# Kernel tuning notes

Measured on AMD Instinct MI355X. Metric: run time of the kernel, lower is better.

Reference implementation:

```python
import jax, jax.numpy as jnp
import numpy as np


def setup_inputs() -> dict:
    key = jax.random.key(0)
    k1, k2, k3 = jax.random.split(key, 3)
    B, C, H, W = 4, 32, 256, 256
    nw, nh = 16, 16
    K = nw * nh
    pixel_feats = jax.random.normal(k1, (B, C, H, W), dtype=jnp.float32)
    assoc_map = jax.random.uniform(k2, (B, 9, H, W), dtype=jnp.float32)
    index_map = jax.random.randint(k3, (B, H, W), 0, K, dtype=jnp.int32)
    return {
        "pixel_feats": pixel_feats,
        "assoc_map": assoc_map,
        "index_map": index_map,
        "nw_spixels": nw,
        "nh_spixels": nh,
    }


def reference(pixel_feats, assoc_map, index_map, nw_spixels, nh_spixels):
    # pixel_feats: [B,C,H,W], assoc_map: [B,9,H,W] (3x3 superpixel-neighbor
    # association weights, row-major (dy,dx) in {-1,0,1}^2), index_map: [B,H,W]
    # base superpixel id in [0, nw*nh). Output: [B, C, nw*nh].
    B, C, H, W = pixel_feats.shape
    K = nw_spixels * nh_spixels
    P = H * W

    idx = index_map.reshape(B, P).astype(jnp.int32)
    ix = idx % nw_spixels  # base spixel grid x
    iy = idx // nw_spixels  # base spixel grid y

    # 9 relative offsets over the superpixel grid
    dy, dx = jnp.meshgrid(jnp.arange(-1, 2), jnp.arange(-1, 2), indexing="ij")
    dy = dy.reshape(9)
    dx = dx.reshape(9)

    tx = ix[:, None, :] + dx[None, :, None]  # [B,9,P]
    ty = iy[:, None, :] + dy[None, :, None]
    valid = (tx >= 0) & (tx < nw_spixels) & (ty >= 0) & (ty < nh_spixels)
    tgt = jnp.where(valid, ty * nw_spixels + tx, 0)  # [B,9,P]

    w = assoc_map.reshape(B, 9, P) * valid.astype(assoc_map.dtype)  # [B,9,P]

    # fold batch into segment id so a single segment_sum handles all images
    seg = (tgt + jnp.arange(B, dtype=jnp.int32)[:, None, None] * K).reshape(-1)

    wsum = jax.ops.segment_sum(w.reshape(-1), seg, num_segments=B * K)  # [B*K]

    # weighted pixel features scattered into superpixel bins
    contrib = w[:, :, None, :] * pixel_feats.reshape(B, 1, C, P)  # [B,9,C,P]
    contrib = contrib.transpose(0, 1, 3, 2).reshape(-1, C)  # [B*9*P, C]
    fsum = jax.ops.segment_sum(contrib, seg, num_segments=B * K)  # [B*K, C]

    eps = 1e-16
    denom = jnp.where(wsum > eps, wsum, 1.0)
    sp = jnp.where(wsum[:, None] > eps, fsum / denom[:, None], 0.0)
    return sp.reshape(B, K, C).transpose(0, 2, 1)  # [B,C,K]
```

## Files before the change

kernel.cpp:

```cpp
#include <hip/hip_runtime.h>
#include <hip/hip_bf16.h>


#define CCH  32
#define TPB  1024
#define PPB  1024
#define STPB 512
#define CAPC 384
#define RECW 24
#define CNTS 16
#define KMAX 256

__device__ __forceinline__ unsigned pack_bf16(float a, float b) {
    unsigned ua = __float_as_uint(a);
    unsigned ub = __float_as_uint(b);
    ua = (ua + 0x7FFFu + ((ua >> 16) & 1u)) >> 16;
    ub = (ub + 0x7FFFu + ((ub >> 16) & 1u)) >> 16;
    return ua | (ub << 16);
}
__device__ __forceinline__ float bf_lo(unsigned u) {
    return __uint_as_float(u << 16);
}
__device__ __forceinline__ float bf_hi(unsigned u) {
    return __uint_as_float(u & 0xFFFF0000u);
}

__global__ __launch_bounds__(TPB) void spx_prep_kernel(
    const float* __restrict__ pf,
    const float* __restrict__ assoc,
    const int*   __restrict__ idxmap,
    const int*   __restrict__ nw_p,
    const int*   __restrict__ nh_p,
    int*         __restrict__ cnt,
    unsigned*    __restrict__ recs,
    float*       __restrict__ ovf,
    int P, int K, int cap, int bpb)
{
    __shared__ int hist[KMAX];
    __shared__ int bases[KMAX];

    const int b   = blockIdx.x / bpb;
    const int blk = blockIdx.x - b * bpb;
    const int tid = threadIdx.x;
    const int p   = blk * PPB + tid;

    if (tid < KMAX) hist[tid] = 0;
    __syncthreads();

    const int*   ix_b = idxmap + (size_t)b * P;
    const float* pf_b = pf     + (size_t)b * CCH * P;
    const float* as_b = assoc  + (size_t)b * 9 * P;

    const int idx  = ix_b[p];
    const int rank = atomicAdd(&hist[idx], 1);

    unsigned u[16];
#pragma unroll
    for (int c2 = 0; c2 < 16; ++c2) {
        const float f0 = pf_b[(size_t)(2*c2  ) * P + p];
        const float f1 = pf_b[(size_t)(2*c2+1) * P + p];
        u[c2] = pack_bf16(f0, f1);
    }
    float wv[9];
#pragma unroll
    for (int j = 0; j < 9; ++j) wv[j] = as_b[(size_t)j * P + p];

    __syncthreads();
    if (tid < KMAX)
        bases[tid] = atomicAdd(&cnt[(b * K + tid) * CNTS], hist[tid]);
    __syncthreads();

    const int pos = bases[idx] + rank;

    if (pos < cap) {
        unsigned* dst = recs + ((size_t)(b * K + idx) * cap + pos) * RECW;
        uint4* d4 = (uint4*)dst;
        d4[0] = make_uint4(u[0],  u[1],  u[2],  u[3]);
        d4[1] = make_uint4(u[4],  u[5],  u[6],  u[7]);
        d4[2] = make_uint4(u[8],  u[9],  u[10], u[11]);
        d4[3] = make_uint4(u[12], u[13], u[14], u[15]);
        d4[4] = make_uint4(pack_bf16(wv[0], wv[1]), pack_bf16(wv[2], wv[3]),
                           pack_bf16(wv[4], wv[5]), pack_bf16(wv[6], wv[7]));
        dst[20] = pack_bf16(wv[8], 0.0f);
    } else {
        const int nw = nw_p[0], nh = nh_p[0];
        const int iy = idx / nw, ixx = idx - (idx / nw) * nw;
#pragma unroll
        for (int j = 0; j < 9; ++j) {
            const int ty = iy + j / 3 - 1, tx = ixx + j % 3 - 1;
            if (tx >= 0 && tx < nw && ty >= 0 && ty < nh) {
                float* o = ovf + (size_t)(b * K + ty * nw + tx) * (CCH + 1);
#pragma unroll
                for (int c2 = 0; c2 < 16; ++c2) {
                    unsafeAtomicAdd(&o[2*c2],     wv[j] * bf_lo(u[c2]));
                    unsafeAtomicAdd(&o[2*c2 + 1], wv[j] * bf_hi(u[c2]));
                }
                unsafeAtomicAdd(&o[CCH], wv[j]);
            }
        }
    }
}

__global__ __launch_bounds__(STPB) void spx_scan_kernel(
    const unsigned* __restrict__ recs,
    const int*      __restrict__ cnt,
    float*          __restrict__ partial,
    int K, int cap)
{
    __shared__ float red[32][9][CCH + 1];

    const int bs  = blockIdx.x;
    const int tid = threadIdx.x;
    const int c2  = tid & 15;
    const int g   = tid >> 4;

    int c = cnt[bs * CNTS];
    if (c > cap) c = cap;
    const unsigned* rb = recs + (size_t)bs * cap * RECW;

    float a[9][2];
    float wa = 0.f;
#pragma unroll
    for (int j = 0; j < 9; ++j) { a[j][0] = 0.f; a[j][1] = 0.f; }

    for (int i = g; i < c; i += 32) {
        const unsigned* r = rb + (size_t)i * RECW;
        const unsigned uf  = r[c2];
        const float f0 = bf_lo(uf), f1 = bf_hi(uf);
        const unsigned wp0 = r[16], wp1 = r[17], wp2 = r[18],
                       wp3 = r[19], wp4 = r[20];
        const float w[9] = { bf_lo(wp0), bf_hi(wp0), bf_lo(wp1), bf_hi(wp1),
                             bf_lo(wp2), bf_hi(wp2), bf_lo(wp3), bf_hi(wp3),
                             bf_lo(wp4) };
#pragma unroll
        for (int j = 0; j < 9; ++j) {
            a[j][0] += w[j] * f0;
            a[j][1] += w[j] * f1;
        }
        wa += w[0] + w[1] + w[2] + w[3] + w[4] + w[5] + w[6] + w[7] + w[8];
    }

    (void)wa;

    float ws[9];
#pragma unroll
    for (int j = 0; j < 9; ++j) ws[j] = 0.f;
    if (c2 == 0) {
        for (int i = g; i < c; i += 32) {
            const unsigned* r = rb + (size_t)i * RECW;
            const unsigned wp0 = r[16], wp1 = r[17], wp2 = r[18],
                           wp3 = r[19], wp4 = r[20];
            ws[0] += bf_lo(wp0); ws[1] += bf_hi(wp0);
            ws[2] += bf_lo(wp1); ws[3] += bf_hi(wp1);
            ws[4] += bf_lo(wp2); ws[5] += bf_hi(wp2);
            ws[6] += bf_lo(wp3); ws[7] += bf_hi(wp3);
            ws[8] += bf_lo(wp4);
        }
    }

#pragma unroll
    for (int j = 0; j < 9; ++j) {
        red[g][j][2 * c2]     = a[j][0];
        red[g][j][2 * c2 + 1] = a[j][1];
    }
    if (c2 == 0) {
#pragma unroll
        for (int j = 0; j < 9; ++j) red[g][j][CCH] = ws[j];
    }
    __syncthreads();

    float* pout = partial + (size_t)bs * 9 * (CCH + 1);
    for (int col = tid; col < 9 * (CCH + 1); col += STPB) {
        const int j  = col / (CCH + 1);
        const int cc = col - j * (CCH + 1);
        float s = 0.f;
#pragma unroll
        for (int g2 = 0; g2 < 32; ++g2) s += red[g2][j][cc];
        pout[col] = s;
    }
}

__global__ __launch_bounds__(64) void spx_finalize_kernel(
    const float* __restrict__ partial,
    const float* __restrict__ ovf,
    const int*   __restrict__ nw_p,
    const int*   __restrict__ nh_p,
    float*       __restrict__ out,
    int K)
{
    __shared__ float F[CCH + 1];

    const int b   = blockIdx.x / K;
    const int k   = blockIdx.x - b * K;
    const int tid = threadIdx.x;
    const int nw  = nw_p[0];
    const int nh  = nh_p[0];
    const int ky  = k / nw;
    const int kx  = k - ky * nw;

    if (tid < CCH + 1) {
        float s = ovf[(size_t)(b * K + k) * (CCH + 1) + tid];
#pragma unroll
        for (int j = 0; j < 9; ++j) {
            const int dy = j / 3 - 1, dx = j % 3 - 1;
            const int sy = ky - dy, sx = kx - dx;
            if (sx >= 0 && sx < nw && sy >= 0 && sy < nh) {
                s += partial[((size_t)(b * K + sy * nw + sx) * 9 + j)
                             * (CCH + 1) + tid];
            }
        }
        F[tid] = s;
    }
    __syncthreads();

    if (tid < CCH) {
        const float W = F[CCH];
        out[((size_t)b * CCH + tid) * K + k] =
            (W > 1e-16f) ? (F[tid] / W) : 0.f;
    }
}

extern "C" void kernel_launch(void* const* d_in, const int* in_sizes, int n_in,
                              void* d_out, int out_size, void* d_ws, size_t ws_size,
                              hipStream_t stream) {
    const float* pf     = (const float*)d_in[0];
    const float* assoc  = (const float*)d_in[1];
    const int*   idxmap = (const int*)d_in[2];
    const int*   nw_p   = (const int*)d_in[3];
    const int*   nh_p   = (const int*)d_in[4];
    float* out = (float*)d_out;

    const int BP = in_sizes[2];
    const int B  = 4;
    const int P  = BP / B;
    const int K  = out_size / (B * CCH);

    const size_t cnt_bytes  = (size_t)B * K * CNTS * sizeof(int);
    const size_t ovf_bytes  = (size_t)B * K * (CCH + 1) * sizeof(float);
    const size_t part_bytes = (size_t)B * K * 9 * (CCH + 1) * sizeof(float);
    int*      cnt     = (int*)d_ws;
    float*    ovf     = (float*)((char*)d_ws + cnt_bytes);
    float*    partial = (float*)((char*)d_ws + cnt_bytes + ovf_bytes);
    unsigned* recs    = (unsigned*)((char*)d_ws + cnt_bytes + ovf_bytes
                                    + part_bytes);

    size_t used = cnt_bytes + ovf_bytes + part_bytes;
    size_t avail = (ws_size > used) ? (ws_size - used) : 0;
    int cap = (int)(avail / ((size_t)B * K * RECW * sizeof(unsigned)));
    if (cap > CAPC) cap = CAPC;
    if (cap < 1) cap = 1;

    hipMemsetAsync(cnt, 0, cnt_bytes + ovf_bytes, stream);

    const int bpb = P / PPB;
    spx_prep_kernel<<<B * bpb, TPB, 0, stream>>>(
        pf, assoc, idxmap, nw_p, nh_p, cnt, recs, ovf, P, K, cap, bpb);

    spx_scan_kernel<<<B * K, STPB, 0, stream>>>(recs, cnt, partial, K, cap);

    spx_finalize_kernel<<<B * K, 64, 0, stream>>>(
        partial, ovf, nw_p, nh_p, out, K);
}
```

Measured before the change: 112.4 us.

## Split prep into rank and fill kernels; fold weight sums into main scan loop

The combined prep kernel is split in two. A light 1024-thread rank kernel reads only the index map and computes each pixel's slot. A separate 256-thread fill kernel then loads features and weights and writes the bf16 records, so the heavy loads no longer sit inside a block that syncs twice. The scan kernel now accumulates the per-neighbor weight sums inside its main loop instead of rereading the records in a second pass on one lane per group. The split adds a kernel launch and a slot array round-trip through global memory. The overflow path now reloads fp32 features instead of using the packed bf16 values.

```diff
diff --git a/kernel.cpp b/kernel.cpp
--- a/kernel.cpp
+++ b/kernel.cpp
@@ -3,8 +3,8 @@
 
 
 #define CCH  32
-#define TPB  1024
-#define PPB  1024
+#define RTPB 1024
+#define FTPB 256
 #define STPB 512
 #define CAPC 384
 #define RECW 24
@@ -25,15 +25,10 @@
     return __uint_as_float(u & 0xFFFF0000u);
 }
 
-__global__ __launch_bounds__(TPB) void spx_prep_kernel(
-    const float* __restrict__ pf,
-    const float* __restrict__ assoc,
-    const int*   __restrict__ idxmap,
-    const int*   __restrict__ nw_p,
-    const int*   __restrict__ nh_p,
-    int*         __restrict__ cnt,
-    unsigned*    __restrict__ recs,
-    float*       __restrict__ ovf,
+__global__ __launch_bounds__(RTPB) void spx_rank_kernel(
+    const int* __restrict__ idxmap,
+    int*       __restrict__ cnt,
+    int*       __restrict__ slot,
     int P, int K, int cap, int bpb)
 {
     __shared__ int hist[KMAX];
@@ -42,17 +37,39 @@
     const int b   = blockIdx.x / bpb;
     const int blk = blockIdx.x - b * bpb;
     const int tid = threadIdx.x;
-    const int p   = blk * PPB + tid;
+    const int p   = blk * RTPB + tid;
 
     if (tid < KMAX) hist[tid] = 0;
     __syncthreads();
 
-    const int*   ix_b = idxmap + (size_t)b * P;
-    const float* pf_b = pf     + (size_t)b * CCH * P;
-    const float* as_b = assoc  + (size_t)b * 9 * P;
-
-    const int idx  = ix_b[p];
+    const int idx  = idxmap[(size_t)b * P + p];
     const int rank = atomicAdd(&hist[idx], 1);
+    __syncthreads();
+
+    if (tid < KMAX)
+        bases[tid] = atomicAdd(&cnt[(b * K + tid) * CNTS], hist[tid]);
+    __syncthreads();
+
+    const int pos = bases[idx] + rank;
+    const int bkt = b * K + idx;
+    slot[(size_t)b * P + p] = (pos < cap) ? (bkt * cap + pos) : -(bkt + 1);
+}
+
+__global__ __launch_bounds__(FTPB) void spx_fill_kernel(
+    const float* __restrict__ pf,
+    const float* __restrict__ assoc,
+    const int*   __restrict__ slot,
+    const int*   __restrict__ nw_p,
+    const int*   __restrict__ nh_p,
+    unsigned*    __restrict__ recs,
+    float*       __restrict__ ovf,
+    int P, int K, int cpb)
+{
+    const int b = blockIdx.x / cpb;
+    const int p = (blockIdx.x - b * cpb) * FTPB + threadIdx.x;
+
+    const float* pf_b = pf    + (size_t)b * CCH * P;
+    const float* as_b = assoc + (size_t)b * 9 * P;
 
     unsigned u[16];
 #pragma unroll
@@ -65,15 +82,10 @@
 #pragma unroll
     for (int j = 0; j < 9; ++j) wv[j] = as_b[(size_t)j * P + p];
 
-    __syncthreads();
-    if (tid < KMAX)
-        bases[tid] = atomicAdd(&cnt[(b * K + tid) * CNTS], hist[tid]);
-    __syncthreads();
-
-    const int pos = bases[idx] + rank;
-
-    if (pos < cap) {
-        unsigned* dst = recs + ((size_t)(b * K + idx) * cap + pos) * RECW;
+    const int s = slot[(size_t)b * P + p];
+
+    if (s >= 0) {
+        unsigned* dst = recs + (size_t)s * RECW;
         uint4* d4 = (uint4*)dst;
         d4[0] = make_uint4(u[0],  u[1],  u[2],  u[3]);
         d4[1] = make_uint4(u[4],  u[5],  u[6],  u[7]);
@@ -83,6 +95,8 @@
                            pack_bf16(wv[4], wv[5]), pack_bf16(wv[6], wv[7]));
         dst[20] = pack_bf16(wv[8], 0.0f);
     } else {
+        const int bkt = -s - 1;
+        const int idx = bkt - b * K;
         const int nw = nw_p[0], nh = nh_p[0];
         const int iy = idx / nw, ixx = idx - (idx / nw) * nw;
 #pragma unroll
@@ -92,8 +106,10 @@
                 float* o = ovf + (size_t)(b * K + ty * nw + tx) * (CCH + 1);
 #pragma unroll
                 for (int c2 = 0; c2 < 16; ++c2) {
-                    unsafeAtomicAdd(&o[2*c2],     wv[j] * bf_lo(u[c2]));
-                    unsafeAtomicAdd(&o[2*c2 + 1], wv[j] * bf_hi(u[c2]));
+                    const float f0 = pf_b[(size_t)(2*c2  ) * P + p];
+                    const float f1 = pf_b[(size_t)(2*c2+1) * P + p];
+                    unsafeAtomicAdd(&o[2*c2],     wv[j] * f0);
+                    unsafeAtomicAdd(&o[2*c2 + 1], wv[j] * f1);
                 }
                 unsafeAtomicAdd(&o[CCH], wv[j]);
             }
@@ -118,10 +134,9 @@
     if (c > cap) c = cap;
     const unsigned* rb = recs + (size_t)bs * cap * RECW;
 
-    float a[9][2];
-    float wa = 0.f;
-#pragma unroll
-    for (int j = 0; j < 9; ++j) { a[j][0] = 0.f; a[j][1] = 0.f; }
+    float a[9][2], ws[9];
+#pragma unroll
+    for (int j = 0; j < 9; ++j) { a[j][0] = 0.f; a[j][1] = 0.f; ws[j] = 0.f; }
 
     for (int i = g; i < c; i += 32) {
         const unsigned* r = rb + (size_t)i * RECW;
@@ -136,25 +151,7 @@
         for (int j = 0; j < 9; ++j) {
             a[j][0] += w[j] * f0;
             a[j][1] += w[j] * f1;
-        }
-        wa += w[0] + w[1] + w[2] + w[3] + w[4] + w[5] + w[6] + w[7] + w[8];
-    }
-
-    (void)wa;
-
-    float ws[9];
-#pragma unroll
-    for (int j = 0; j < 9; ++j) ws[j] = 0.f;
-    if (c2 == 0) {
-        for (int i = g; i < c; i += 32) {
-            const unsigned* r = rb + (size_t)i * RECW;
-            const unsigned wp0 = r[16], wp1 = r[17], wp2 = r[18],
-                           wp3 = r[19], wp4 = r[20];
-            ws[0] += bf_lo(wp0); ws[1] += bf_hi(wp0);
-            ws[2] += bf_lo(wp1); ws[3] += bf_hi(wp1);
-            ws[4] += bf_lo(wp2); ws[5] += bf_hi(wp2);
-            ws[6] += bf_lo(wp3); ws[7] += bf_hi(wp3);
-            ws[8] += bf_lo(wp4);
+            ws[j]   += w[j];
         }
     }
 
@@ -238,23 +235,30 @@
     const size_t cnt_bytes  = (size_t)B * K * CNTS * sizeof(int);
     const size_t ovf_bytes  = (size_t)B * K * (CCH + 1) * sizeof(float);
     const size_t part_bytes = (size_t)B * K * 9 * (CCH + 1) * sizeof(float);
+    const size_t slot_bytes = (size_t)BP * sizeof(int);
     int*      cnt     = (int*)d_ws;
     float*    ovf     = (float*)((char*)d_ws + cnt_bytes);
     float*    partial = (float*)((char*)d_ws + cnt_bytes + ovf_bytes);
+    int*      slot    = (int*)((char*)d_ws + cnt_bytes + ovf_bytes
+                               + part_bytes);
     unsigned* recs    = (unsigned*)((char*)d_ws + cnt_bytes + ovf_bytes
-                                    + part_bytes);
-
-    size_t used = cnt_bytes + ovf_bytes + part_bytes;
-    size_t avail = (ws_size > used) ? (ws_size - used) : 0;
+                                    + part_bytes + slot_bytes);
+
+    const size_t used  = cnt_bytes + ovf_bytes + part_bytes + slot_bytes;
+    const size_t avail = (ws_size > used) ? (ws_size - used) : 0;
     int cap = (int)(avail / ((size_t)B * K * RECW * sizeof(unsigned)));
     if (cap > CAPC) cap = CAPC;
     if (cap < 1) cap = 1;
 
     hipMemsetAsync(cnt, 0, cnt_bytes + ovf_bytes, stream);
 
-    const int bpb = P / PPB;
-    spx_prep_kernel<<<B * bpb, TPB, 0, stream>>>(
-        pf, assoc, idxmap, nw_p, nh_p, cnt, recs, ovf, P, K, cap, bpb);
+    const int bpb = P / RTPB;
+    spx_rank_kernel<<<B * bpb, RTPB, 0, stream>>>(
+        idxmap, cnt, slot, P, K, cap, bpb);
+
+    const int cpb = P / FTPB;
+    spx_fill_kernel<<<B * cpb, FTPB, 0, stream>>>(
+        pf, assoc, slot, nw_p, nh_p, recs, ovf, P, K, cpb);
 
     spx_scan_kernel<<<B * K, STPB, 0, stream>>>(recs, cnt, partial, K, cap);
 
```

New measurement: 116.0 us. 1.03x slower.

## Scatter scan partials via atomics into fsum, drop partial buffer, simplify finalize

Applied to the files above, without the earlier changes.

The scan kernel now atomically adds each block's 9 neighbor partial sums straight into the shared fsum/overflow accumulator, so the separate partial buffer and the 9-way gather in finalize go away. The weight-sum accumulation is folded into the main scan loop instead of a second pass over the records by c2==0 threads. Finalize becomes a flat elementwise divide with coalesced output writes, and prep gets a min-blocks launch-bounds hint. The cost is global float atomics with contention (up to 9 writers per bin) and ordering-dependent float rounding.

```diff
diff --git a/kernel.cpp b/kernel.cpp
--- a/kernel.cpp
+++ b/kernel.cpp
@@ -25,7 +25,7 @@
     return __uint_as_float(u & 0xFFFF0000u);
 }
 
-__global__ __launch_bounds__(TPB) void spx_prep_kernel(
+__global__ __launch_bounds__(TPB, 4) void spx_prep_kernel(
     const float* __restrict__ pf,
     const float* __restrict__ assoc,
     const int*   __restrict__ idxmap,
@@ -33,7 +33,7 @@
     const int*   __restrict__ nh_p,
     int*         __restrict__ cnt,
     unsigned*    __restrict__ recs,
-    float*       __restrict__ ovf,
+    float*       __restrict__ fsum,
     int P, int K, int cap, int bpb)
 {
     __shared__ int hist[KMAX];
@@ -89,7 +89,7 @@
         for (int j = 0; j < 9; ++j) {
             const int ty = iy + j / 3 - 1, tx = ixx + j % 3 - 1;
             if (tx >= 0 && tx < nw && ty >= 0 && ty < nh) {
-                float* o = ovf + (size_t)(b * K + ty * nw + tx) * (CCH + 1);
+                float* o = fsum + (size_t)(b * K + ty * nw + tx) * (CCH + 1);
 #pragma unroll
                 for (int c2 = 0; c2 < 16; ++c2) {
                     unsafeAtomicAdd(&o[2*c2],     wv[j] * bf_lo(u[c2]));
@@ -104,7 +104,9 @@
 __global__ __launch_bounds__(STPB) void spx_scan_kernel(
     const unsigned* __restrict__ recs,
     const int*      __restrict__ cnt,
-    float*          __restrict__ partial,
+    const int*      __restrict__ nw_p,
+    const int*      __restrict__ nh_p,
+    float*          __restrict__ fsum,
     int K, int cap)
 {
     __shared__ float red[32][9][CCH + 1];
@@ -118,10 +120,9 @@
     if (c > cap) c = cap;
     const unsigned* rb = recs + (size_t)bs * cap * RECW;
 
-    float a[9][2];
-    float wa = 0.f;
-#pragma unroll
-    for (int j = 0; j < 9; ++j) { a[j][0] = 0.f; a[j][1] = 0.f; }
+    float a[9][2], ws9[9];
+#pragma unroll
+    for (int j = 0; j < 9; ++j) { a[j][0] = 0.f; a[j][1] = 0.f; ws9[j] = 0.f; }
 
     for (int i = g; i < c; i += 32) {
         const unsigned* r = rb + (size_t)i * RECW;
@@ -136,25 +137,7 @@
         for (int j = 0; j < 9; ++j) {
             a[j][0] += w[j] * f0;
             a[j][1] += w[j] * f1;
-        }
-        wa += w[0] + w[1] + w[2] + w[3] + w[4] + w[5] + w[6] + w[7] + w[8];
-    }
-
-    (void)wa;
-
-    float ws[9];
-#pragma unroll
-    for (int j = 0; j < 9; ++j) ws[j] = 0.f;
-    if (c2 == 0) {
-        for (int i = g; i < c; i += 32) {
-            const unsigned* r = rb + (size_t)i * RECW;
-            const unsigned wp0 = r[16], wp1 = r[17], wp2 = r[18],
-                           wp3 = r[19], wp4 = r[20];
-            ws[0] += bf_lo(wp0); ws[1] += bf_hi(wp0);
-            ws[2] += bf_lo(wp1); ws[3] += bf_hi(wp1);
-            ws[4] += bf_lo(wp2); ws[5] += bf_hi(wp2);
-            ws[6] += bf_lo(wp3); ws[7] += bf_hi(wp3);
-            ws[8] += bf_lo(wp4);
+            ws9[j]  += w[j];
         }
     }
 
@@ -165,59 +148,44 @@
     }
     if (c2 == 0) {
 #pragma unroll
-        for (int j = 0; j < 9; ++j) red[g][j][CCH] = ws[j];
-    }
-    __syncthreads();
-
-    float* pout = partial + (size_t)bs * 9 * (CCH + 1);
+        for (int j = 0; j < 9; ++j) red[g][j][CCH] = ws9[j];
+    }
+    __syncthreads();
+
+    const int b  = bs / K;
+    const int s  = bs - b * K;
+    const int nw = nw_p[0];
+    const int nh = nh_p[0];
+    const int sy = s / nw;
+    const int sx = s - sy * nw;
+
     for (int col = tid; col < 9 * (CCH + 1); col += STPB) {
         const int j  = col / (CCH + 1);
         const int cc = col - j * (CCH + 1);
-        float s = 0.f;
-#pragma unroll
-        for (int g2 = 0; g2 < 32; ++g2) s += red[g2][j][cc];
-        pout[col] = s;
-    }
-}
-
-__global__ __launch_bounds__(64) void spx_finalize_kernel(
-    const float* __restrict__ partial,
-    const float* __restrict__ ovf,
-    const int*   __restrict__ nw_p,
-    const int*   __restrict__ nh_p,
+        const int ty = sy + j / 3 - 1;
+        const int tx = sx + j % 3 - 1;
+        if (tx < 0 || tx >= nw || ty < 0 || ty >= nh) continue;
+        float sum = 0.f;
+#pragma unroll
+        for (int g2 = 0; g2 < 32; ++g2) sum += red[g2][j][cc];
+        unsafeAtomicAdd(&fsum[(size_t)(b * K + ty * nw + tx) * (CCH + 1) + cc],
+                        sum);
+    }
+}
+
+__global__ __launch_bounds__(256) void spx_finalize_kernel(
+    const float* __restrict__ fsum,
     float*       __restrict__ out,
-    int K)
+    int K, int total)
 {
-    __shared__ float F[CCH + 1];
-
-    const int b   = blockIdx.x / K;
-    const int k   = blockIdx.x - b * K;
-    const int tid = threadIdx.x;
-    const int nw  = nw_p[0];
-    const int nh  = nh_p[0];
-    const int ky  = k / nw;
-    const int kx  = k - ky * nw;
-
-    if (tid < CCH + 1) {
-        float s = ovf[(size_t)(b * K + k) * (CCH + 1) + tid];
-#pragma unroll
-        for (int j = 0; j < 9; ++j) {
-            const int dy = j / 3 - 1, dx = j % 3 - 1;
-            const int sy = ky - dy, sx = kx - dx;
-            if (sx >= 0 && sx < nw && sy >= 0 && sy < nh) {
-                s += partial[((size_t)(b * K + sy * nw + sx) * 9 + j)
-                             * (CCH + 1) + tid];
-            }
-        }
-        F[tid] = s;
-    }
-    __syncthreads();
-
-    if (tid < CCH) {
-        const float W = F[CCH];
-        out[((size_t)b * CCH + tid) * K + k] =
-            (W > 1e-16f) ? (F[tid] / W) : 0.f;
-    }
+    const int gid = blockIdx.x * 256 + threadIdx.x;
+    if (gid >= total) return;
+    const int k = gid % K;
+    const int c = (gid / K) % CCH;
+    const int b = gid / (K * CCH);
+    const float* f = fsum + (size_t)(b * K + k) * (CCH + 1);
+    const float W = f[CCH];
+    out[gid] = (W > 1e-16f) ? (f[c] / W) : 0.f;
 }
 
 extern "C" void kernel_launch(void* const* d_in, const int* in_sizes, int n_in,
@@ -236,28 +204,27 @@
     const int K  = out_size / (B * CCH);
 
     const size_t cnt_bytes  = (size_t)B * K * CNTS * sizeof(int);
-    const size_t ovf_bytes  = (size_t)B * K * (CCH + 1) * sizeof(float);
-    const size_t part_bytes = (size_t)B * K * 9 * (CCH + 1) * sizeof(float);
-    int*      cnt     = (int*)d_ws;
-    float*    ovf     = (float*)((char*)d_ws + cnt_bytes);
-    float*    partial = (float*)((char*)d_ws + cnt_bytes + ovf_bytes);
-    unsigned* recs    = (unsigned*)((char*)d_ws + cnt_bytes + ovf_bytes
-                                    + part_bytes);
-
-    size_t used = cnt_bytes + ovf_bytes + part_bytes;
-    size_t avail = (ws_size > used) ? (ws_size - used) : 0;
+    const size_t fsum_bytes = (size_t)B * K * (CCH + 1) * sizeof(float);
+    int*      cnt  = (int*)d_ws;
+    float*    fsum = (float*)((char*)d_ws + cnt_bytes);
+    unsigned* recs = (unsigned*)((char*)d_ws + cnt_bytes + fsum_bytes);
+
+    const size_t used  = cnt_bytes + fsum_bytes;
+    const size_t avail = (ws_size > used) ? (ws_size - used) : 0;
     int cap = (int)(avail / ((size_t)B * K * RECW * sizeof(unsigned)));
     if (cap > CAPC) cap = CAPC;
     if (cap < 1) cap = 1;
 
-    hipMemsetAsync(cnt, 0, cnt_bytes + ovf_bytes, stream);
+    hipMemsetAsync(cnt, 0, cnt_bytes + fsum_bytes, stream);
 
     const int bpb = P / PPB;
     spx_prep_kernel<<<B * bpb, TPB, 0, stream>>>(
-        pf, assoc, idxmap, nw_p, nh_p, cnt, recs, ovf, P, K, cap, bpb);
-
-    spx_scan_kernel<<<B * K, STPB, 0, stream>>>(recs, cnt, partial, K, cap);
-
-    spx_finalize_kernel<<<B * K, 64, 0, stream>>>(
-        partial, ovf, nw_p, nh_p, out, K);
-}
+        pf, assoc, idxmap, nw_p, nh_p, cnt, recs, fsum, P, K, cap, bpb);
+
+    spx_scan_kernel<<<B * K, STPB, 0, stream>>>(
+        recs, cnt, nw_p, nh_p, fsum, K, cap);
+
+    const int total = B * K * CCH;
+    spx_finalize_kernel<<<(total + 255) / 256, 256, 0, stream>>>(
+        fsum, out, K, total);
+}
```

New measurement: 109.9 us. 2.2% less time.
